# Optimization experiments

Hardware: AMD Instinct MI355X
Metric: run time of the kernel (lower is better)

Reference implementation:

```python
import jax, jax.numpy as jnp
import numpy as np

N, P, CF, K = 64, 1024, 16, 16  # batch, points, feature channels (after stripping 2 coord dims), knn K
BN_EPS = 1e-5


def _bn(x, g, b, m, v):
    # channel-last batchnorm in eval mode
    return (x - m) / jnp.sqrt(v + BN_EPS) * g + b


def _knn(pts, k):
    # pts: (N,P,2) -> indices of k nearest neighbors excluding self: (N,P,k)
    r = jnp.sum(pts * pts, axis=-1)                      # (N,P)
    d = r[:, :, None] - 2.0 * jnp.einsum('npc,nqc->npq', pts, pts) + r[:, None, :]
    _, idx = jax.lax.top_k(-d, k + 1)                    # (N,P,k+1)
    return idx[:, :, 1:]


def setup_inputs() -> dict:
    key = jax.random.key(0)
    ks = jax.random.split(key, 8)
    inp = {
        'features': jax.random.normal(ks[0], (N, P, 2 + CF), dtype=jnp.float32),
        'mask': jnp.zeros((N, P), dtype=bool),
        # edge conv stack: Conv2d(32->64), Conv2d(64->64), Conv2d(64->64), all 1x1
        'W0': jax.random.normal(ks[1], (64, 2 * CF), dtype=jnp.float32) / np.sqrt(2 * CF),
        'W1': jax.random.normal(ks[2], (64, 64), dtype=jnp.float32) / 8.0,
        'W2': jax.random.normal(ks[3], (64, 64), dtype=jnp.float32) / 8.0,
        # shortcut Conv1d(16->64)
        'Ws': jax.random.normal(ks[4], (64, CF), dtype=jnp.float32) / np.sqrt(CF),
    }
    for i, kk in zip(['0', '1', '2', 's'], jax.random.split(ks[5], 4)):
        k1, k2 = jax.random.split(kk)
        inp['g' + i] = jnp.ones((64,), jnp.float32)
        inp['b' + i] = jnp.zeros((64,), jnp.float32)
        inp['m' + i] = 0.1 * jax.random.normal(k1, (64,), jnp.float32)
        inp['v' + i] = jnp.ones((64,), jnp.float32) + 0.1 * jax.random.uniform(k2, (64,))
    return inp


def reference(features, mask, W0, W1, W2, Ws,
              g0, b0, m0, v0, g1, b1, m1, v1, g2, b2, m2, v2, gs, bs, ms, vs):
    pts = features[..., :2]          # (N,P,2)
    X = features[..., 2:]            # (N,P,CF)
    X_shortcut = X

    idx = _knn(pts, K)               # (N,P,K)
    f = jax.vmap(lambda x, i: x[i])(X, idx)              # gather neighbors: (N,P,K,CF)
    fc = jnp.broadcast_to(X[:, :, None, :], f.shape)     # center tiled
    h = jnp.concatenate([fc, fc - f], axis=-1)           # (N,P,K,2*CF)

    valid = mask.shape[1] - jnp.sum(mask, axis=1)        # (N,) number of valid points
    mask_K = idx >= valid[:, None, None]                 # (N,P,K) neighbor is padding

    for W, g, b, m, v in ((W0, g0, b0, m0, v0), (W1, g1, b1, m1, v1), (W2, g2, b2, m2, v2)):
        h = jax.nn.relu(_bn(jnp.einsum('npkc,oc->npko', h, W), g, b, m, v))

    h = jnp.where(mask_K[..., None], 0.0, h)             # (N,P,K,64)
    denom = jnp.maximum((K - jnp.sum(mask_K, axis=2)).astype(h.dtype), 1e-8)[..., None]
    agg = jnp.sum(h, axis=2) / denom                     # masked mean over K: (N,P,64)

    sc = _bn(jnp.einsum('npc,oc->npo', X_shortcut, Ws), gs, bs, ms, vs)
    sc = jnp.where(mask[..., None], 0.0, sc)

    out = jax.nn.relu(agg + sc)                          # (N,P,64)
    return jnp.transpose(out, (0, 2, 1))                 # (N,64,P) to match torch layout
```

## Files before the change

kernel.cpp:

```cpp
#include <hip/hip_runtime.h>

#define N_P 1024
#define N_K 16
#define C_IN 18

typedef _Float16 f16;
typedef f16 f16x8 __attribute__((ext_vector_type(8)));
typedef f16 f16x4 __attribute__((ext_vector_type(4)));
typedef float f32x4 __attribute__((ext_vector_type(4)));

__global__ __launch_bounds__(256, 3) void fused_kernel(
    const float* __restrict__ feat, const unsigned char* __restrict__ mask,
    const float* __restrict__ W0, const float* __restrict__ W1,
    const float* __restrict__ W2, const float* __restrict__ Ws,
    const float* __restrict__ g0, const float* __restrict__ b0,
    const float* __restrict__ m0, const float* __restrict__ v0,
    const float* __restrict__ g1, const float* __restrict__ b1,
    const float* __restrict__ m1, const float* __restrict__ v1,
    const float* __restrict__ g2, const float* __restrict__ b2,
    const float* __restrict__ m2, const float* __restrict__ v2,
    const float* __restrict__ gs, const float* __restrict__ bs,
    const float* __restrict__ ms, const float* __restrict__ vs,
    float* __restrict__ out) {

    __shared__ __align__(16) char sbytes[16640 + 9216 + 4096 + 16];
    float4* spts = (float4*)sbytes;
    float (*fbuf)[65] = (float(*)[65])sbytes;
    f16 (*hb)[16][72] = (f16(*)[16][72])(sbytes + 16640);
    int (*idx_lds)[16] = (int(*)[16])(sbytes + 16640 + 9216);
    int* msum = (int*)(sbytes + 16640 + 9216 + 4096);

    const int tid = threadIdx.x;
    const int lane = tid & 63;
    const int w = tid >> 6;
    const int g = lane >> 4;
    const int c15 = lane & 15;
    const int n = blockIdx.x >> 4;
    const int P0 = (blockIdx.x & 15) << 6;
    const int PB = P0 + (w << 4);

    const float* fB = feat + (size_t)n * N_P * C_IN;

    if (tid == 0) *msum = 0;
    __syncthreads();
    for (int i = tid; i < N_P; i += 256) {
        float x = fB[i * C_IN + 0];
        float y = fB[i * C_IN + 1];
        float r = __fadd_rn(__fmul_rn(x, x), __fmul_rn(y, y));
        spts[i] = make_float4(x, y, r, 0.f);
    }
    {
        unsigned int m4 = *(const unsigned int*)(mask + (size_t)n * N_P + tid * 4);
        int mc = (int)(((m4 & 0xFFu) != 0) + (((m4 >> 8) & 0xFFu) != 0) +
                       (((m4 >> 16) & 0xFFu) != 0) + (((m4 >> 24) & 0xFFu) != 0));
        atomicAdd(msum, mc);
    }
    __syncthreads();
    const int valid = N_P - *msum;

    double kk[17];
    {
        const int qid = c15;
        const int s = g;
        const int base = s << 8;
        const float4 me = spts[P0 + (w << 4) + qid];
        const float px = me.x, py = me.y, rp = me.z;

#pragma unroll
        for (int j = 0; j < 17; ++j) kk[j] = 0x1.0p60;

        int off = (2 * s) & 255;
        float4 nq = spts[base + off];
        for (int i = 0; i < 256; ++i) {
            const float4 qc = nq;
            const int cur = base + off;
            off = (off + 1) & 255;
            nq = spts[base + off];
            float dot = __fadd_rn(__fmul_rn(px, qc.x), __fmul_rn(py, qc.y));
            float d   = __fadd_rn(__builtin_fmaf(-2.f, dot, rp), qc.z);
            unsigned int ud = __float_as_uint(d);
            ud ^= (unsigned int)((int)ud >> 31) | 0x80000000u;
            double x = __builtin_fma((double)ud, 1024.0, (double)cur);
#pragma unroll
            for (int j = 0; j < 17; ++j) {
                double lo = fmin(kk[j], x);
                x = fmax(kk[j], x);
                kk[j] = lo;
            }
        }
#pragma unroll
        for (int r = 0; r < 2; ++r) {
            const int m = (r == 0) ? 32 : 16;
            const bool recv = (lane & m) == 0;
#pragma unroll
            for (int j = 0; j < 17; ++j) {
                double x = __shfl_xor(kk[j], m, 64);
                x = recv ? x : __builtin_inf();
#pragma unroll
                for (int jj = 0; jj < 17; ++jj) {
                    double lo = fmin(kk[jj], x);
                    x = fmax(kk[jj], x);
                    kk[jj] = lo;
                }
            }
        }
        if (lane < 16) {
            const int row = (w << 4) + qid;
#pragma unroll
            for (int j = 1; j < 17; ++j) {
                double hi = __builtin_trunc(kk[j] * 0x1.0p-10);
                idx_lds[row][j - 1] = (int)(kk[j] - hi * 1024.0);
            }
        }
    }
    __syncthreads();

    float tb0[4], tb1[4], tb2[4], tbs[4];
    f16x8 w0f[4], w1f[4][2], w2f[4][2];
    f16x4 wsf[4];
#pragma unroll
    for (int t = 0; t < 4; ++t) {
        const int o = t * 16 + c15;
        float s0 = g0[o] / sqrtf(v0[o] + 1e-5f);  tb0[t] = b0[o] - m0[o] * s0;
        float s1 = g1[o] / sqrtf(v1[o] + 1e-5f);  tb1[t] = b1[o] - m1[o] * s1;
        float s2 = g2[o] / sqrtf(v2[o] + 1e-5f);  tb2[t] = b2[o] - m2[o] * s2;
        float ss = gs[o] / sqrtf(vs[o] + 1e-5f);  tbs[t] = bs[o] - ms[o] * ss;
        const float* w0r = W0 + o * 32 + g * 8;
#pragma unroll
        for (int e = 0; e < 8; ++e) w0f[t][e] = (f16)(w0r[e] * s0);
        const float* w1r = W1 + o * 64 + g * 8;
        const float* w2r = W2 + o * 64 + g * 8;
#pragma unroll
        for (int ch = 0; ch < 2; ++ch)
#pragma unroll
            for (int e = 0; e < 8; ++e) {
                w1f[t][ch][e] = (f16)(w1r[ch * 32 + e] * s1);
                w2f[t][ch][e] = (f16)(w2r[ch * 32 + e] * s2);
            }
        const float* wsr = Ws + o * 16 + g * 4;
#pragma unroll
        for (int e = 0; e < 4; ++e) wsf[t][e] = (f16)(wsr[e] * ss);
    }

    for (int pp = 0; pp < 16; ++pp) {
        const int p = PB + pp;
        const int* ip = idx_lds[(w << 4) + pp];

        const int q = ip[c15];
        const int half = g & 1;
        const float* fcp = fB + p * C_IN + 2 + half * 8;
        float e0[8];
#pragma unroll
        for (int j = 0; j < 4; ++j) {
            float2 v = *(const float2*)(fcp + 2 * j);
            e0[2 * j] = v.x; e0[2 * j + 1] = v.y;
        }
        if (g >= 2) {
            const float* fqp = fB + q * C_IN + 2 + half * 8;
#pragma unroll
            for (int j = 0; j < 4; ++j) {
                float2 v = *(const float2*)(fqp + 2 * j);
                e0[2 * j] -= v.x; e0[2 * j + 1] -= v.y;
            }
        }
        f16x8 a0;
#pragma unroll
        for (int j = 0; j < 8; ++j) a0[j] = (f16)e0[j];

        f32x4 acc[4];
#pragma unroll
        for (int t = 0; t < 4; ++t) {
            acc[t] = (f32x4){tb0[t], tb0[t], tb0[t], tb0[t]};
            acc[t] = __builtin_amdgcn_mfma_f32_16x16x32_f16(a0, w0f[t], acc[t], 0, 0, 0);
        }
#pragma unroll
        for (int t = 0; t < 4; ++t)
#pragma unroll
            for (int r = 0; r < 4; ++r)
                hb[w][4 * g + r][t * 16 + c15] = (f16)fmaxf(acc[t][r], 0.f);

        f16x8 a1a = *(const f16x8*)&hb[w][c15][g * 8];
        f16x8 a1b = *(const f16x8*)&hb[w][c15][32 + g * 8];
        f32x4 acc1[4];
#pragma unroll
        for (int t = 0; t < 4; ++t) {
            acc1[t] = (f32x4){tb1[t], tb1[t], tb1[t], tb1[t]};
            acc1[t] = __builtin_amdgcn_mfma_f32_16x16x32_f16(a1a, w1f[t][0], acc1[t], 0, 0, 0);
            acc1[t] = __builtin_amdgcn_mfma_f32_16x16x32_f16(a1b, w1f[t][1], acc1[t], 0, 0, 0);
        }
#pragma unroll
        for (int t = 0; t < 4; ++t)
#pragma unroll
            for (int r = 0; r < 4; ++r)
                hb[w][4 * g + r][t * 16 + c15] = (f16)fmaxf(acc1[t][r], 0.f);

        f16x8 a2a = *(const f16x8*)&hb[w][c15][g * 8];
        f16x8 a2b = *(const f16x8*)&hb[w][c15][32 + g * 8];
        f32x4 acc2[4];
#pragma unroll
        for (int t = 0; t < 4; ++t) {
            acc2[t] = (f32x4){tb2[t], tb2[t], tb2[t], tb2[t]};
            acc2[t] = __builtin_amdgcn_mfma_f32_16x16x32_f16(a2a, w2f[t][0], acc2[t], 0, 0, 0);
            acc2[t] = __builtin_amdgcn_mfma_f32_16x16x32_f16(a2b, w2f[t][1], acc2[t], 0, 0, 0);
        }
        float ssum[4] = {0.f, 0.f, 0.f, 0.f};
        int cnt = 0;
#pragma unroll
        for (int r = 0; r < 4; ++r) {
            int qq = ip[4 * g + r];
            bool fl = (qq >= valid);
            cnt += fl ? 1 : 0;
#pragma unroll
            for (int t = 0; t < 4; ++t) {
                float v = fmaxf(acc2[t][r], 0.f);
                ssum[t] += fl ? 0.f : v;
            }
        }
#pragma unroll
        for (int t = 0; t < 4; ++t) {
            ssum[t] += __shfl_xor(ssum[t], 16);
            ssum[t] += __shfl_xor(ssum[t], 32);
        }
        cnt += __shfl_xor(cnt, 16);
        cnt += __shfl_xor(cnt, 32);
        float dn = fmaxf((float)(N_K - cnt), 1e-8f);
        if (g == 0) {
            int prow = (w << 4) + pp;
#pragma unroll
            for (int t = 0; t < 4; ++t)
                fbuf[prow][t * 16 + c15] = ssum[t] / dn;
        }
    }

    {
        const float* xr = fB + (size_t)(PB + c15) * C_IN + 2 + g * 4;
        float2 xa = *(const float2*)(xr);
        float2 xb = *(const float2*)(xr + 2);
        f16x4 as;
        as[0] = (f16)xa.x; as[1] = (f16)xa.y; as[2] = (f16)xb.x; as[3] = (f16)xb.y;
        f32x4 sacc[4];
#pragma unroll
        for (int t = 0; t < 4; ++t) {
            sacc[t] = (f32x4){tbs[t], tbs[t], tbs[t], tbs[t]};
            sacc[t] = __builtin_amdgcn_mfma_f32_16x16x16f16(as, wsf[t], sacc[t], 0, 0, 0);
        }
        const unsigned char* mrow = mask + (size_t)n * N_P + P0;
#pragma unroll
        for (int r = 0; r < 4; ++r) {
            int pl = (w << 4) + 4 * g + r;
            bool mk = (mrow[pl] != 0);
#pragma unroll
            for (int t = 0; t < 4; ++t) {
                float a = fbuf[pl][t * 16 + c15];
                float sv = mk ? 0.f : sacc[t][r];
                fbuf[pl][t * 16 + c15] = fmaxf(a + sv, 0.f);
            }
        }
    }
    __syncthreads();

    float* ob = out + (size_t)n * 64 * N_P + P0;
#pragma unroll
    for (int oo = 0; oo < 16; ++oo) {
        int o = (w << 4) + oo;
        ob[(size_t)o * N_P + lane] = fbuf[lane][o];
    }
}

extern "C" void kernel_launch(void* const* d_in, const int* in_sizes, int n_in,
                              void* d_out, int out_size, void* d_ws, size_t ws_size,
                              hipStream_t stream) {
    (void)in_sizes; (void)n_in; (void)out_size; (void)d_ws; (void)ws_size;
    const float* feat = (const float*)d_in[0];
    const unsigned char* mask = (const unsigned char*)d_in[1];
    const float* W0 = (const float*)d_in[2];
    const float* W1 = (const float*)d_in[3];
    const float* W2 = (const float*)d_in[4];
    const float* Ws = (const float*)d_in[5];
    const float* g0 = (const float*)d_in[6];
    const float* b0 = (const float*)d_in[7];
    const float* m0 = (const float*)d_in[8];
    const float* v0 = (const float*)d_in[9];
    const float* g1 = (const float*)d_in[10];
    const float* b1 = (const float*)d_in[11];
    const float* m1 = (const float*)d_in[12];
    const float* v1 = (const float*)d_in[13];
    const float* g2 = (const float*)d_in[14];
    const float* b2 = (const float*)d_in[15];
    const float* m2 = (const float*)d_in[16];
    const float* v2 = (const float*)d_in[17];
    const float* gs = (const float*)d_in[18];
    const float* bs = (const float*)d_in[19];
    const float* ms = (const float*)d_in[20];
    const float* vs = (const float*)d_in[21];
    float* out = (float*)d_out;

    fused_kernel<<<1024, 256, 0, stream>>>(feat, mask, W0, W1, W2, Ws,
                                           g0, b0, m0, v0, g1, b1, m1, v1,
                                           g2, b2, m2, v2, gs, bs, ms, vs,
                                           out);
}
```

Measured before the change: 295.1 us.

## Split KNN into float threshold pass plus candidate compaction and double merge

Replaces the single double-precision 17-entry insertion-sort KNN scan with two passes. The first pass uses float min/max to find the 17th-smallest distance threshold per query. The second pass recomputes distances and pushes only candidates at or below the threshold into a shared-memory list via atomics. A final double-key sort over at most 25 candidates then recovers the indices. This aims to cut the cost of double fmin/fmax in the hot loop, but it adds a second scan, shared atomics, and a cap of 25 candidates that could drop neighbours when many distances tie.

```diff
diff --git a/kernel.cpp b/kernel.cpp
--- a/kernel.cpp
+++ b/kernel.cpp
@@ -23,12 +23,14 @@
     const float* __restrict__ ms, const float* __restrict__ vs,
     float* __restrict__ out) {
 
-    __shared__ __align__(16) char sbytes[16640 + 9216 + 4096 + 16];
+    __shared__ __align__(16) char sbytes[30224];
     float4* spts = (float4*)sbytes;
     float (*fbuf)[65] = (float(*)[65])sbytes;
+    double (*items)[25] = (double(*)[25])(sbytes + 16640);
     f16 (*hb)[16][72] = (f16(*)[16][72])(sbytes + 16640);
     int (*idx_lds)[16] = (int(*)[16])(sbytes + 16640 + 9216);
-    int* msum = (int*)(sbytes + 16640 + 9216 + 4096);
+    int* cnt = (int*)(sbytes + 29952);
+    int* msum = (int*)(sbytes + 30208);
 
     const int tid = threadIdx.x;
     const int lane = tid & 63;
@@ -42,6 +44,7 @@
     const float* fB = feat + (size_t)n * N_P * C_IN;
 
     if (tid == 0) *msum = 0;
+    if (tid < 64) cnt[tid] = 0;
     __syncthreads();
     for (int i = tid; i < N_P; i += 256) {
         float x = fB[i * C_IN + 0];
@@ -58,18 +61,59 @@
     __syncthreads();
     const int valid = N_P - *msum;
 
-    double kk[17];
-    {
-        const int qid = c15;
-        const int s = g;
-        const int base = s << 8;
-        const float4 me = spts[P0 + (w << 4) + qid];
-        const float px = me.x, py = me.y, rp = me.z;
-
-#pragma unroll
-        for (int j = 0; j < 17; ++j) kk[j] = 0x1.0p60;
-
-        int off = (2 * s) & 255;
+    const int qid = c15;
+    const int qrow = (w << 4) + qid;
+    const int base = g << 8;
+
+    float px, py, rp;
+    {
+        const float4 me = spts[P0 + qrow];
+        px = me.x; py = me.y; rp = me.z;
+    }
+
+    float tau;
+    {
+        float kd[17];
+#pragma unroll
+        for (int j = 0; j < 17; ++j) kd[j] = __builtin_inff();
+
+        int off = (2 * g) & 255;
+        float4 nq = spts[base + off];
+        for (int i = 0; i < 256; ++i) {
+            const float4 qc = nq;
+            off = (off + 1) & 255;
+            nq = spts[base + off];
+            float dot = __fadd_rn(__fmul_rn(px, qc.x), __fmul_rn(py, qc.y));
+            float d   = __fadd_rn(__builtin_fmaf(-2.f, dot, rp), qc.z);
+            float x = d;
+#pragma unroll
+            for (int j = 0; j < 17; ++j) {
+                float lo = fminf(kd[j], x);
+                x = fmaxf(kd[j], x);
+                kd[j] = lo;
+            }
+        }
+#pragma unroll
+        for (int r = 0; r < 2; ++r) {
+            const int m = (r == 0) ? 32 : 16;
+            const bool recv = (lane & m) == 0;
+#pragma unroll
+            for (int j = 0; j < 17; ++j) {
+                float x = __shfl_xor(kd[j], m, 64);
+                x = recv ? x : __builtin_inff();
+#pragma unroll
+                for (int jj = 0; jj < 17; ++jj) {
+                    float lo = fminf(kd[jj], x);
+                    x = fmaxf(kd[jj], x);
+                    kd[jj] = lo;
+                }
+            }
+        }
+        tau = __shfl(kd[16], c15);
+    }
+
+    {
+        int off = (2 * g) & 255;
         float4 nq = spts[base + off];
         for (int i = 0; i < 256; ++i) {
             const float4 qc = nq;
@@ -78,42 +122,41 @@
             nq = spts[base + off];
             float dot = __fadd_rn(__fmul_rn(px, qc.x), __fmul_rn(py, qc.y));
             float d   = __fadd_rn(__builtin_fmaf(-2.f, dot, rp), qc.z);
-            unsigned int ud = __float_as_uint(d);
-            ud ^= (unsigned int)((int)ud >> 31) | 0x80000000u;
-            double x = __builtin_fma((double)ud, 1024.0, (double)cur);
-#pragma unroll
-            for (int j = 0; j < 17; ++j) {
-                double lo = fmin(kk[j], x);
-                x = fmax(kk[j], x);
-                kk[j] = lo;
-            }
-        }
-#pragma unroll
-        for (int r = 0; r < 2; ++r) {
-            const int m = (r == 0) ? 32 : 16;
-            const bool recv = (lane & m) == 0;
-#pragma unroll
-            for (int j = 0; j < 17; ++j) {
-                double x = __shfl_xor(kk[j], m, 64);
-                x = recv ? x : __builtin_inf();
-#pragma unroll
-                for (int jj = 0; jj < 17; ++jj) {
-                    double lo = fmin(kk[jj], x);
-                    x = fmax(kk[jj], x);
-                    kk[jj] = lo;
-                }
-            }
-        }
-        if (lane < 16) {
-            const int row = (w << 4) + qid;
-#pragma unroll
-            for (int j = 1; j < 17; ++j) {
-                double hi = __builtin_trunc(kk[j] * 0x1.0p-10);
-                idx_lds[row][j - 1] = (int)(kk[j] - hi * 1024.0);
-            }
-        }
-    }
-    __syncthreads();
+            if (d <= tau) {
+                unsigned int ud = __float_as_uint(d);
+                ud ^= (unsigned int)((int)ud >> 31) | 0x80000000u;
+                double key = __builtin_fma((double)ud, 1024.0, (double)cur);
+                int slot = atomicAdd(&cnt[qrow], 1);
+                if (slot < 25) items[qrow][slot] = key;
+            }
+        }
+    }
+    __syncthreads();
+
+    double kk[17];
+#pragma unroll
+    for (int j = 0; j < 17; ++j) kk[j] = 0x1.0p60;
+    if (lane < 16) {
+        const int c = min(cnt[qrow], 25);
+        for (int j = 0; j < c; ++j) {
+            double x = items[qrow][j];
+#pragma unroll
+            for (int jj = 0; jj < 17; ++jj) {
+                double lo = fmin(kk[jj], x);
+                x = fmax(kk[jj], x);
+                kk[jj] = lo;
+            }
+        }
+    }
+    __syncthreads();
+
+    if (lane < 16) {
+#pragma unroll
+        for (int j = 1; j < 17; ++j) {
+            double hi = __builtin_trunc(kk[j] * 0x1.0p-10);
+            idx_lds[qrow][j - 1] = (int)(kk[j] - hi * 1024.0);
+        }
+    }
 
     float tb0[4], tb1[4], tb2[4], tbs[4];
     f16x8 w0f[4], w1f[4][2], w2f[4][2];
@@ -204,12 +247,12 @@
             acc2[t] = __builtin_amdgcn_mfma_f32_16x16x32_f16(a2b, w2f[t][1], acc2[t], 0, 0, 0);
         }
         float ssum[4] = {0.f, 0.f, 0.f, 0.f};
-        int cnt = 0;
+        int cnt2 = 0;
 #pragma unroll
         for (int r = 0; r < 4; ++r) {
             int qq = ip[4 * g + r];
             bool fl = (qq >= valid);
-            cnt += fl ? 1 : 0;
+            cnt2 += fl ? 1 : 0;
 #pragma unroll
             for (int t = 0; t < 4; ++t) {
                 float v = fmaxf(acc2[t][r], 0.f);
@@ -221,9 +264,9 @@
             ssum[t] += __shfl_xor(ssum[t], 16);
             ssum[t] += __shfl_xor(ssum[t], 32);
         }
-        cnt += __shfl_xor(cnt, 16);
-        cnt += __shfl_xor(cnt, 32);
-        float dn = fmaxf((float)(N_K - cnt), 1e-8f);
+        cnt2 += __shfl_xor(cnt2, 16);
+        cnt2 += __shfl_xor(cnt2, 32);
+        float dn = fmaxf((float)(N_K - cnt2), 1e-8f);
         if (g == 0) {
             int prow = (w << 4) + pp;
 #pragma unroll
```

After: 319.6 us. 1.08x slower.
